# Performance work log

Hardware: AMD Instinct MI355X
Metric: run time of the kernel (lower is better)

The kernel has to match this reference:

```python
import jax, jax.numpy as jnp
import numpy as np

L, B, E, H, HID = 2048, 4, 512, 8, 2048
HD = E // H


def setup_inputs() -> dict:
    key = jax.random.key(0)
    ks = jax.random.split(key, 6)
    s = 0.02
    x = jax.random.normal(ks[0], (L, B, E), jnp.float32)
    in_proj_w = jax.random.normal(ks[1], (3 * E, E), jnp.float32) * s
    in_proj_b = jnp.zeros((3 * E,), jnp.float32)
    out_w = jax.random.normal(ks[2], (E, E), jnp.float32) * s
    out_b = jnp.zeros((E,), jnp.float32)
    w1 = jax.random.normal(ks[3], (HID, E), jnp.float32) * s  # torch Linear: (out, in)
    b1 = jnp.zeros((HID,), jnp.float32)
    w2 = jax.random.normal(ks[4], (E, HID), jnp.float32) * s
    b2 = jnp.zeros((E,), jnp.float32)
    ln_g = jnp.ones((E,), jnp.float32)
    ln_b = jnp.zeros((E,), jnp.float32)
    return {"x": x, "in_proj_w": in_proj_w, "in_proj_b": in_proj_b,
            "out_w": out_w, "out_b": out_b, "w1": w1, "b1": b1,
            "w2": w2, "b2": b2, "ln_g": ln_g, "ln_b": ln_b}


def _pos_encoding(S, Emb, dtype):
    # even i: sin((t+1) * 10000^(-i/E)); odd i: cos((t+1) * 10000^(-(i+1)/E))
    t = jnp.arange(S, dtype=dtype)[:, None]
    i = jnp.arange(Emb, dtype=dtype)[None, :]
    even = jnp.sin((t + 1.0) * jnp.power(10000.0, -i / Emb))
    odd = jnp.cos((t + 1.0) * jnp.power(10000.0, -(i + 1.0) / Emb))
    return jnp.where(jnp.arange(Emb)[None, :] % 2 == 0, even, odd)  # (S, Emb)


def _layernorm(x, g, b, eps=1e-5):
    mu = jnp.mean(x, axis=-1, keepdims=True)
    var = jnp.mean(jnp.square(x - mu), axis=-1, keepdims=True)
    return (x - mu) * jax.lax.rsqrt(var + eps) * g + b


def _mha(x, in_proj_w, in_proj_b, out_w, out_b):
    # x: (L, B, E); self-attention, torch MultiheadAttention semantics
    qkv = jnp.einsum('lbe,fe->lbf', x, in_proj_w) + in_proj_b
    q, k, v = jnp.split(qkv, 3, axis=-1)
    q = q.reshape(L, B, H, HD)
    k = k.reshape(L, B, H, HD)
    v = v.reshape(L, B, H, HD)
    scores = jnp.einsum('lbhd,mbhd->bhlm', q, k) / np.sqrt(HD).astype(np.float32)
    attn = jax.nn.softmax(scores, axis=-1)
    o = jnp.einsum('bhlm,mbhd->lbhd', attn, v).reshape(L, B, E)
    return jnp.einsum('lbe,fe->lbf', o, out_w) + out_b


def reference(x, in_proj_w, in_proj_b, out_w, out_b, w1, b1, w2, b2, ln_g, ln_b):
    # positional encoding: varies along dim1, broadcasts along dim0 (as in source)
    pe = _pos_encoding(x.shape[1], x.shape[2], x.dtype)  # (B, E)
    x = x + pe[None, :, :]
    # Post-Norm path
    x = _layernorm(_mha(x, in_proj_w, in_proj_b, out_w, out_b) + x, ln_g, ln_b)
    h = jax.nn.gelu(jnp.einsum('lbe,he->lbh', x, w1) + b1, approximate=False)
    ff = jnp.einsum('lbh,eh->lbe', h, w2) + b2
    x = _layernorm(ff + x, ln_g, ln_b)
    return x
```

## Files before the change

kernel.cpp:

```cpp
#include <hip/hip_runtime.h>

typedef unsigned short u16;
typedef unsigned int   u32;
typedef u16  u16x2 __attribute__((ext_vector_type(2)));
typedef u16  u16x4 __attribute__((ext_vector_type(4)));
typedef u16  u16x8 __attribute__((ext_vector_type(8)));
typedef short s8v  __attribute__((ext_vector_type(8)));
typedef float f4v  __attribute__((ext_vector_type(4)));
typedef u32  u32x2 __attribute__((ext_vector_type(2)));
typedef u32  u32x4 __attribute__((ext_vector_type(4)));

#define L_SEQ 2048
#define B_SZ  4
#define E_DIM 512
#define H_CNT 8
#define HD    64
#define HID   2048
#define M_ROWS (L_SEQ * B_SZ)
#define QSCALE 0.18033688011112042f

__device__ __forceinline__ u16 f2b(float f) {
    unsigned u = __builtin_bit_cast(unsigned, f);
    u += 0x7fffu + ((u >> 16) & 1u);
    return (u16)(u >> 16);
}
__device__ __forceinline__ float b2f(u16 u) {
    u32 x = ((u32)u) << 16; return __builtin_bit_cast(float, x);
}
#if defined(__has_builtin)
#if __has_builtin(__builtin_amdgcn_cvt_pk_bf16_f32)
#define HAVE_PK_BF16 1
#endif
#if __has_builtin(__builtin_amdgcn_rcpf)
#define HAVE_RCPF 1
#endif
#endif
__device__ __forceinline__ u32 pk_trunc(float a, float b) {
#ifdef HAVE_PK_BF16
    typedef __bf16 bf2 __attribute__((ext_vector_type(2)));
    bf2 r = __builtin_amdgcn_cvt_pk_bf16_f32(a, b);
    return __builtin_bit_cast(u32, r);
#else
    u32 ua = __builtin_bit_cast(u32, a), ub = __builtin_bit_cast(u32, b);
    return (ua >> 16) | (ub & 0xffff0000u);
#endif
}
__device__ __forceinline__ float frcp(float x) {
#ifdef HAVE_RCPF
    return __builtin_amdgcn_rcpf(x);
#else
    return 1.0f / x;
#endif
}
__device__ __forceinline__ void gload_lds16(const u16* g, u16* l) {
    __builtin_amdgcn_global_load_lds((__attribute__((address_space(1))) void*)(u16*)g,
                                     (__attribute__((address_space(3))) void*)l, 16, 0, 0);
}
__device__ __forceinline__ float gelu_f(float v) {
    float y2 = v * (1.5957691216f + 0.0713548576f * v * v);
    return v / (1.0f + __expf(-y2));
}

__global__ __launch_bounds__(256) void pe_tab_k(float* __restrict__ pet) {
    int i = blockIdx.x * 256 + threadIdx.x;
    int e = i & (E_DIM - 1);
    float t = (float)(i >> 9) + 1.0f;
    int ee = (e & 1) ? (e + 1) : e;
    float w = exp2f((-(float)ee / 512.0f) * 13.287712379549449f);
    pet[i] = (e & 1) ? cosf(t * w) : sinf(t * w);
}

__global__ __launch_bounds__(256) void pe_add_k(const float* __restrict__ x,
                                                const float* __restrict__ pet,
                                                u16* __restrict__ xpb) {
    int idx = (blockIdx.x * 256 + threadIdx.x) * 4;
    f4v v = *(const f4v*)(x + idx);
    f4v p = *(const f4v*)(pet + (idx & 2047));
    u16x4 o;
#pragma unroll
    for (int i = 0; i < 4; ++i) o[i] = f2b(v[i] + p[i]);
    *(u16x4*)(xpb + idx) = o;
}

__global__ __launch_bounds__(256) void conv4_k(const float* __restrict__ s1, u16* __restrict__ d1, int n1,
                                               const float* __restrict__ s2, u16* __restrict__ d2, int n2,
                                               const float* __restrict__ s3, u16* __restrict__ d3, int n3,
                                               const float* __restrict__ s4, u16* __restrict__ d4) {
    int o = (blockIdx.x * 256 + threadIdx.x) * 4;
    const float* s; u16* d;
    if (o < n1) { s = s1; d = d1; }
    else { o -= n1;
        if (o < n2) { s = s2; d = d2; }
        else { o -= n2;
            if (o < n3) { s = s3; d = d3; }
            else { o -= n3; s = s4; d = d4; } } }
    f4v v = *(const f4v*)(s + o);
    u16x4 q;
#pragma unroll
    for (int i = 0; i < 4; ++i) q[i] = f2b(v[i]);
    *(u16x4*)(d + o) = q;
}

template <int NP, bool WRITEF, bool WRITEB>
__global__ __launch_bounds__(256)
void ln_c(const u16* __restrict__ p0, const u16* __restrict__ p1,
          const u16* __restrict__ p2, const u16* __restrict__ p3,
          const float* __restrict__ bias, const u16* __restrict__ resid,
          const float* __restrict__ gw, const float* __restrict__ bw,
          float* __restrict__ outF, u16* __restrict__ outB) {
    int wave = threadIdx.x >> 6, lane = threadIdx.x & 63;
    size_t row = (size_t)blockIdx.x * 4 + wave;
    size_t off = row * E_DIM + lane * 8;
    u16x8 rv = *(const u16x8*)(resid + off);
    f4v a, b;
#pragma unroll
    for (int i = 0; i < 4; ++i) { a[i] = b2f(rv[i]); b[i] = b2f(rv[i + 4]); }
    a += *(const f4v*)(bias + lane * 8);
    b += *(const f4v*)(bias + lane * 8 + 4);
    const u16* ps[4] = {p0, p1, p2, p3};
#pragma unroll
    for (int z = 0; z < NP; ++z) {
        u16x8 t = *(const u16x8*)(ps[z] + off);
#pragma unroll
        for (int i = 0; i < 4; ++i) { a[i] += b2f(t[i]); b[i] += b2f(t[i + 4]); }
    }
    float s = (a[0] + a[1]) + (a[2] + a[3]) + (b[0] + b[1]) + (b[2] + b[3]);
#pragma unroll
    for (int o = 1; o < 64; o <<= 1) s += __shfl_xor(s, o, 64);
    float mu = s * (1.0f / E_DIM);
    float q = 0.f;
#pragma unroll
    for (int i = 0; i < 4; ++i) { float d = a[i] - mu; q += d * d; }
#pragma unroll
    for (int i = 0; i < 4; ++i) { float d = b[i] - mu; q += d * d; }
#pragma unroll
    for (int o = 1; o < 64; o <<= 1) q += __shfl_xor(q, o, 64);
    float rstd = rsqrtf(q * (1.0f / E_DIM) + 1e-5f);
    f4v g0 = *(const f4v*)(gw + lane * 8), g1 = *(const f4v*)(gw + lane * 8 + 4);
    f4v w0 = *(const f4v*)(bw + lane * 8), w1 = *(const f4v*)(bw + lane * 8 + 4);
    f4v y0, y1;
#pragma unroll
    for (int i = 0; i < 4; ++i) { y0[i] = (a[i] - mu) * rstd * g0[i] + w0[i];
                                  y1[i] = (b[i] - mu) * rstd * g1[i] + w1[i]; }
    if (WRITEF) {
        *(f4v*)(outF + off)     = y0;
        *(f4v*)(outF + off + 4) = y1;
    }
    if (WRITEB) {
        u16x8 o;
#pragma unroll
        for (int i = 0; i < 4; ++i) { o[i] = f2b(y0[i]); o[i + 4] = f2b(y1[i]); }
        *(u16x8*)(outB + off) = o;
    }
}

__global__ __launch_bounds__(256) void transpose_v_k(const u16* __restrict__ vb,
                                                     u16* __restrict__ vt) {
    __shared__ __align__(16) u16 T[64 * 66];
    int t = threadIdx.x;
    int lt = blockIdx.x, bh = blockIdx.y;
    const u16* src = vb + (size_t)bh * (L_SEQ * HD) + (size_t)lt * 64 * HD;
    int lr = t >> 2, d0 = (t & 3) * 16;
    s8v va = *(const s8v*)(src + lr * HD + d0);
    s8v vb8 = *(const s8v*)(src + lr * HD + d0 + 8);
#pragma unroll
    for (int c = 0; c < 4; ++c) {
        u16x2 p0; p0[0] = (u16)va[c * 2]; p0[1] = (u16)va[c * 2 + 1];
        u16x2 p1; p1[0] = (u16)vb8[c * 2]; p1[1] = (u16)vb8[c * 2 + 1];
        *(u16x2*)(&T[lr * 66 + d0 + c * 2])     = p0;
        *(u16x2*)(&T[lr * 66 + d0 + 8 + c * 2]) = p1;
    }
    __syncthreads();
    int d = t >> 2, l0 = (t & 3) * 16;
    u16 tmp[16];
#pragma unroll
    for (int i = 0; i < 16; ++i) tmp[i] = T[(l0 + i) * 66 + d];
    u16* dst = vt + (size_t)bh * (L_SEQ * HD) + (size_t)d * L_SEQ + lt * 64 + l0;
    u16x8 o0, o1;
#pragma unroll
    for (int i = 0; i < 8; ++i) { o0[i] = tmp[i]; o1[i] = tmp[8 + i]; }
    *(u16x8*)dst       = o0;
    *(u16x8*)(dst + 8) = o1;
}

template <int MODE, int NT>
__global__ __launch_bounds__(256, 4)
void gemm_bt(const u16* __restrict__ A, const u16* __restrict__ Bw,
             const float* __restrict__ bias, int M, int N, int K,
             u16* __restrict__ outB,
             u16* __restrict__ oq, u16* __restrict__ okk, u16* __restrict__ ov) {
    __shared__ __align__(16) u16 As[2][128 * 32];
    __shared__ __align__(16) u16 Bs[2][128 * 32];
    const int tid = threadIdx.x;
    const int wave = tid >> 6, lane = tid & 63;
    const int col = lane & 15, quad = lane >> 4;
    const int n = blockIdx.x;
    const int xcd = n & 7, loc = n >> 3;
    const int mpx = (M / 128) >> 3;
    const int bm = (xcd * mpx + loc / NT) * 128;
    const int bn = (loc % NT) * 128;
    const int wm = (wave >> 1) * 64, wn = (wave & 1) * 64;
    f4v acc[4][4] = {};
    const int srow = wave * 16 + (lane >> 2);
    const int soff = (lane & 3) * 8;
    const u16* Ag = A + (size_t)(bm + srow) * K + soff;
    const u16* Bg = Bw + (size_t)(bn + srow) * K + soff;
    const int wo = wave * 512;
    gload_lds16(Ag,                  &As[0][wo]);
    gload_lds16(Ag + (size_t)64 * K, &As[0][wo + 2048]);
    gload_lds16(Bg,                  &Bs[0][wo]);
    gload_lds16(Bg + (size_t)64 * K, &Bs[0][wo + 2048]);
    const int nit = K >> 5;
    for (int t = 0; t < nit; ++t) {
        const int cur = t & 1, nxt = cur ^ 1;
        __syncthreads();
        if (t + 1 < nit) {
            const int kc = (t + 1) * 32;
            gload_lds16(Ag + kc,                  &As[nxt][wo]);
            gload_lds16(Ag + (size_t)64 * K + kc, &As[nxt][wo + 2048]);
            gload_lds16(Bg + kc,                  &Bs[nxt][wo]);
            gload_lds16(Bg + (size_t)64 * K + kc, &Bs[nxt][wo + 2048]);
        }
        s8v af[4], bf[4];
#pragma unroll
        for (int i = 0; i < 4; ++i) af[i] = *(const s8v*)(&As[cur][(wm + i * 16 + col) * 32 + quad * 8]);
#pragma unroll
        for (int j = 0; j < 4; ++j) bf[j] = *(const s8v*)(&Bs[cur][(wn + j * 16 + col) * 32 + quad * 8]);
#pragma unroll
        for (int i = 0; i < 4; ++i)
#pragma unroll
            for (int j = 0; j < 4; ++j)
                acc[i][j] = __builtin_amdgcn_mfma_f32_16x16x32_bf16(af[i], bf[j], acc[i][j], 0, 0, 0);
    }
#pragma unroll
    for (int j = 0; j < 4; ++j) {
        int gn = bn + wn + j * 16 + col;
        float bv = bias[gn];
        int which = gn >> 9, hh = (gn >> 6) & 7, d = gn & 63;
        u16* dst = (MODE == 0) ? ((which == 0) ? oq : ((which == 1) ? okk : ov)) : outB;
        float qs = (MODE == 0 && which == 0) ? QSCALE : 1.0f;
#pragma unroll
        for (int i = 0; i < 4; ++i) {
            int gm0 = bm + wm + i * 16 + quad * 4;
#pragma unroll
            for (int r = 0; r < 4; ++r) {
                float v = acc[i][j][r] + bv;
                int m = gm0 + r;
                if (MODE == 2) {
                    outB[(size_t)m * N + gn] = f2b(gelu_f(v));
                } else {
                    int l = m >> 2, bb = m & 3;
                    dst[((size_t)(bb * H_CNT + hh) * L_SEQ + l) * HD + d] = f2b(v * qs);
                }
            }
        }
    }
}

__global__ __launch_bounds__(256, 4)
void gemm_ks(const u16* __restrict__ A, const u16* __restrict__ Bw,
             int N, int K, int Kper,
             u16* __restrict__ q0, u16* __restrict__ q1) {
    __shared__ __align__(16) u16 As[2][128 * 32];
    __shared__ __align__(16) u16 Bs[2][128 * 32];
    const int tid = threadIdx.x;
    const int wave = tid >> 6, lane = tid & 63;
    const int col = lane & 15, quad = lane >> 4;
    const int n = blockIdx.x;
    const int xcd = n & 7, loc = n >> 3;
    const int bn = (loc & 3) * 128;
    const int bm = (xcd * 8 + ((loc >> 2) & 7)) * 128;
    const int kz = loc >> 5;
    u16* pz = kz ? q1 : q0;
    const int wm = (wave >> 1) * 64, wn = (wave & 1) * 64;
    f4v acc[4][4] = {};
    const int srow = wave * 16 + (lane >> 2);
    const int soff = (lane & 3) * 8;
    const u16* Ag = A + (size_t)(bm + srow) * K + kz * Kper + soff;
    const u16* Bg = Bw + (size_t)(bn + srow) * K + kz * Kper + soff;
    const int wo = wave * 512;
    gload_lds16(Ag,                  &As[0][wo]);
    gload_lds16(Ag + (size_t)64 * K, &As[0][wo + 2048]);
    gload_lds16(Bg,                  &Bs[0][wo]);
    gload_lds16(Bg + (size_t)64 * K, &Bs[0][wo + 2048]);
    const int nit = Kper >> 5;
    for (int t = 0; t < nit; ++t) {
        const int cur = t & 1, nxt = cur ^ 1;
        __syncthreads();
        if (t + 1 < nit) {
            const int kc = (t + 1) * 32;
            gload_lds16(Ag + kc,                  &As[nxt][wo]);
            gload_lds16(Ag + (size_t)64 * K + kc, &As[nxt][wo + 2048]);
            gload_lds16(Bg + kc,                  &Bs[nxt][wo]);
            gload_lds16(Bg + (size_t)64 * K + kc, &Bs[nxt][wo + 2048]);
        }
        s8v af[4], bf[4];
#pragma unroll
        for (int i = 0; i < 4; ++i) af[i] = *(const s8v*)(&As[cur][(wm + i * 16 + col) * 32 + quad * 8]);
#pragma unroll
        for (int j = 0; j < 4; ++j) bf[j] = *(const s8v*)(&Bs[cur][(wn + j * 16 + col) * 32 + quad * 8]);
#pragma unroll
        for (int i = 0; i < 4; ++i)
#pragma unroll
            for (int j = 0; j < 4; ++j)
                acc[i][j] = __builtin_amdgcn_mfma_f32_16x16x32_bf16(af[i], bf[j], acc[i][j], 0, 0, 0);
    }
#pragma unroll
    for (int j = 0; j < 4; ++j) {
        int gn = bn + wn + j * 16 + col;
#pragma unroll
        for (int i = 0; i < 4; ++i) {
            int m0 = bm + wm + i * 16 + quad * 4;
#pragma unroll
            for (int r = 0; r < 4; ++r)
                pz[(size_t)(m0 + r) * N + gn] = f2b(acc[i][j][r]);
        }
    }
}

__global__ __launch_bounds__(256, 4)
void attn_k(const u16* __restrict__ qg, const u16* __restrict__ kg,
            const u16* __restrict__ vtg, u16* __restrict__ og) {
    __shared__ __align__(16) u16 Ks[2][2][64 * 32];
    __shared__ __align__(16) u16 Vs[2][2][64 * 32];
    const int tid = threadIdx.x;
    const int wave = tid >> 6, lane = tid & 63;
    const int col = lane & 15, quad = lane >> 4;
    const int flat = blockIdx.x;
    const int xcd = flat & 7, loc = flat >> 3;
    const int bh = xcd * 4 + (loc >> 4);
    const int qc = loc & 15;
    const size_t base = (size_t)bh * (L_SEQ * HD);
    s8v qf[2][2];
#pragma unroll
    for (int t = 0; t < 2; ++t) {
        const int qrow = qc * 128 + wave * 32 + t * 16 + col;
#pragma unroll
        for (int hh = 0; hh < 2; ++hh)
            qf[t][hh] = *(const s8v*)(qg + base + (size_t)qrow * HD + hh * 32 + quad * 8);
    }
    f4v oa[2][4] = {};
    f4v la[2] = {};
    const s8v vones8 = {0x3F80, 0x3F80, 0x3F80, 0x3F80, 0x3F80, 0x3F80, 0x3F80, 0x3F80};
    const int h = wave & 1, r0 = (wave >> 1) * 16;
    const int srow = lane >> 2, c = lane & 3;
    const int cp = c ^ ((srow >> 1) & 3);
    const int sig = ((srow >> 2) << 3) + ((r0 >> 4) << 2) + (srow & 3);
    const u16* Kg = kg + base + (size_t)sig * HD + h * 32 + cp * 8;
    const u16* Vg = vtg + base + (size_t)(r0 + srow) * L_SEQ + h * 32 + cp * 8;
    {
        gload_lds16(Kg,                      &Ks[0][h][r0 * 32]);
        gload_lds16(Kg + (size_t)32 * HD,    &Ks[0][h][(r0 + 32) * 32]);
        gload_lds16(Vg,                      &Vs[0][h][r0 * 32]);
        gload_lds16(Vg + (size_t)32 * L_SEQ, &Vs[0][h][(r0 + 32) * 32]);
    }
    const int perm = (col >> 1) & 3;
    for (int it = 0; it < 32; ++it) {
        const int cur = it & 1, nxt = cur ^ 1;
        __syncthreads();
        if (it + 1 < 32) {
            const int kv0 = (it + 1) * 64;
            gload_lds16(Kg + (size_t)kv0 * HD,         &Ks[nxt][h][r0 * 32]);
            gload_lds16(Kg + (size_t)(kv0 + 32) * HD,  &Ks[nxt][h][(r0 + 32) * 32]);
            gload_lds16(Vg + kv0,                      &Vs[nxt][h][r0 * 32]);
            gload_lds16(Vg + kv0 + (size_t)32 * L_SEQ, &Vs[nxt][h][(r0 + 32) * 32]);
        }
        f4v st[2][4];
#pragma unroll
        for (int j = 0; j < 4; ++j) {
            s8v k0 = *(const s8v*)(&Ks[cur][0][(j * 16 + col) * 32 + ((quad ^ perm) * 8)]);
            s8v k1 = *(const s8v*)(&Ks[cur][1][(j * 16 + col) * 32 + ((quad ^ perm) * 8)]);
#pragma unroll
            for (int t = 0; t < 2; ++t) {
                f4v z = {};
                z = __builtin_amdgcn_mfma_f32_16x16x32_bf16(k0, qf[t][0], z, 0, 0, 0);
                z = __builtin_amdgcn_mfma_f32_16x16x32_bf16(k1, qf[t][1], z, 0, 0, 0);
                st[t][j] = z;
            }
        }
        u32 pk[2][4][2];
#pragma unroll
        for (int t = 0; t < 2; ++t)
#pragma unroll
            for (int j = 0; j < 4; ++j) {
                f4v p;
#pragma unroll
                for (int r = 0; r < 4; ++r) p[r] = __builtin_amdgcn_exp2f(st[t][j][r]);
                pk[t][j][0] = pk_trunc(p[0], p[1]);
                pk[t][j][1] = pk_trunc(p[2], p[3]);
            }
#pragma unroll
        for (int c2 = 0; c2 < 2; ++c2) {
            s8v pf[2];
#pragma unroll
            for (int t = 0; t < 2; ++t) {
                u32x4 q4 = {pk[t][2 * c2][0], pk[t][2 * c2][1],
                            pk[t][2 * c2 + 1][0], pk[t][2 * c2 + 1][1]};
                pf[t] = __builtin_bit_cast(s8v, q4);
            }
#pragma unroll
            for (int dj = 0; dj < 4; ++dj) {
                s8v vf = *(const s8v*)(&Vs[cur][c2][(dj * 16 + col) * 32 + ((quad ^ perm) * 8)]);
#pragma unroll
                for (int t = 0; t < 2; ++t)
                    oa[t][dj] = __builtin_amdgcn_mfma_f32_16x16x32_bf16(pf[t], vf, oa[t][dj], 0, 0, 0);
            }
#pragma unroll
            for (int t = 0; t < 2; ++t)
                la[t] = __builtin_amdgcn_mfma_f32_16x16x32_bf16(pf[t], vones8, la[t], 0, 0, 0);
        }
    }
    const int b = bh >> 3, hd = bh & 7;
#pragma unroll
    for (int t = 0; t < 2; ++t)
#pragma unroll
        for (int r = 0; r < 4; ++r) {
            float inv = frcp(la[t][r]);
            int lrow = qc * 128 + wave * 32 + t * 16 + quad * 4 + r;
            size_t mrow = (size_t)(lrow * 4 + b) * E_DIM + hd * HD;
#pragma unroll
            for (int dj = 0; dj < 4; ++dj)
                og[mrow + dj * 16 + col] = f2b(oa[t][dj][r] * inv);
        }
}

extern "C" void kernel_launch(void* const* d_in, const int* in_sizes, int n_in,
                              void* d_out, int out_size, void* d_ws, size_t ws_size,
                              hipStream_t stream) {
    const float* x     = (const float*)d_in[0];
    const float* w_qkv = (const float*)d_in[1];
    const float* b_qkv = (const float*)d_in[2];
    const float* w_out = (const float*)d_in[3];
    const float* b_out = (const float*)d_in[4];
    const float* w1    = (const float*)d_in[5];
    const float* b1    = (const float*)d_in[6];
    const float* w2    = (const float*)d_in[7];
    const float* b2    = (const float*)d_in[8];
    const float* ln_g  = (const float*)d_in[9];
    const float* ln_b  = (const float*)d_in[10];

    char* ws = (char*)d_ws;
    u16*   WQKV = (u16*)(ws + 0);
    u16*   WOUT = (u16*)(ws + 1572864);
    u16*   W1B  = (u16*)(ws + 2097152);
    u16*   W2B  = (u16*)(ws + 4194304);
    u16*   XPB  = (u16*)(ws + 6291456);
    u16*   QB   = (u16*)(ws + 14680064);
    u16*   KB   = (u16*)(ws + 23068672);
    u16*   VB   = (u16*)(ws + 31457280);
    u16*   VT   = (u16*)(ws + 39845888);
    float* PET  = (float*)(ws + 82837504);
    u16*   OB   = VB;
    u16*   OP0  = (u16*)(ws + 48234496);
    u16*   OP1  = (u16*)(ws + 56623104);
    u16*   X3B  = QB;
    u16*   HB   = (u16*)(ws + 48234496);
    u16*   FP0  = XPB;
    u16*   FP1  = KB;

    pe_tab_k<<<8, 256, 0, stream>>>(PET);
    pe_add_k<<<4096, 256, 0, stream>>>(x, PET, XPB);
    conv4_k<<<3072, 256, 0, stream>>>(w_qkv, WQKV, 3 * E_DIM * E_DIM,
                                      w_out, WOUT, E_DIM * E_DIM,
                                      w1, W1B, HID * E_DIM,
                                      w2, W2B);
    gemm_bt<0, 12><<<768, 256, 0, stream>>>(XPB, WQKV, b_qkv, M_ROWS, 3 * E_DIM, E_DIM,
                                            nullptr, QB, KB, VB);
    transpose_v_k<<<dim3(32, 32), 256, 0, stream>>>(VB, VT);
    attn_k<<<512, 256, 0, stream>>>(QB, KB, VT, OB);
    gemm_ks<<<512, 256, 0, stream>>>(OB, WOUT, E_DIM, E_DIM, 256, OP0, OP1);
    ln_c<2, false, true><<<2048, 256, 0, stream>>>(OP0, OP1, nullptr, nullptr,
                                                   b_out, XPB, ln_g, ln_b, nullptr, X3B);
    gemm_bt<2, 16><<<1024, 256, 0, stream>>>(X3B, W1B, b1, M_ROWS, HID, E_DIM,
                                             HB, nullptr, nullptr, nullptr);
    gemm_ks<<<512, 256, 0, stream>>>(HB, W2B, E_DIM, HID, 1024, FP0, FP1);
    ln_c<2, true, false><<<2048, 256, 0, stream>>>(FP0, FP1, nullptr, nullptr,
                                                   b2, X3B, ln_g, ln_b, (float*)d_out, nullptr);
}
```

Before: 248.9 us.

## Load attention K/V fragments directly from global into registers, drop LDS staging

```diff
diff --git a/kernel.cpp b/kernel.cpp
--- a/kernel.cpp
+++ b/kernel.cpp
@@ -318,11 +318,9 @@
     }
 }
 
-__global__ __launch_bounds__(256, 4)
+__global__ __launch_bounds__(256, 2)
 void attn_k(const u16* __restrict__ qg, const u16* __restrict__ kg,
             const u16* __restrict__ vtg, u16* __restrict__ og) {
-    __shared__ __align__(16) u16 Ks[2][2][64 * 32];
-    __shared__ __align__(16) u16 Vs[2][2][64 * 32];
     const int tid = threadIdx.x;
     const int wave = tid >> 6, lane = tid & 63;
     const int col = lane & 15, quad = lane >> 4;
@@ -340,82 +338,101 @@
             qf[t][hh] = *(const s8v*)(qg + base + (size_t)qrow * HD + hh * 32 + quad * 8);
     }
     f4v oa[2][4] = {};
-    f4v la[2] = {};
-    const s8v vones8 = {0x3F80, 0x3F80, 0x3F80, 0x3F80, 0x3F80, 0x3F80, 0x3F80, 0x3F80};
-    const int h = wave & 1, r0 = (wave >> 1) * 16;
-    const int srow = lane >> 2, c = lane & 3;
-    const int cp = c ^ ((srow >> 1) & 3);
-    const int sig = ((srow >> 2) << 3) + ((r0 >> 4) << 2) + (srow & 3);
-    const u16* Kg = kg + base + (size_t)sig * HD + h * 32 + cp * 8;
-    const u16* Vg = vtg + base + (size_t)(r0 + srow) * L_SEQ + h * 32 + cp * 8;
-    {
-        gload_lds16(Kg,                      &Ks[0][h][r0 * 32]);
-        gload_lds16(Kg + (size_t)32 * HD,    &Ks[0][h][(r0 + 32) * 32]);
-        gload_lds16(Vg,                      &Vs[0][h][r0 * 32]);
-        gload_lds16(Vg + (size_t)32 * L_SEQ, &Vs[0][h][(r0 + 32) * 32]);
-    }
-    const int perm = (col >> 1) & 3;
-    for (int it = 0; it < 32; ++it) {
-        const int cur = it & 1, nxt = cur ^ 1;
-        __syncthreads();
-        if (it + 1 < 32) {
-            const int kv0 = (it + 1) * 64;
-            gload_lds16(Kg + (size_t)kv0 * HD,         &Ks[nxt][h][r0 * 32]);
-            gload_lds16(Kg + (size_t)(kv0 + 32) * HD,  &Ks[nxt][h][(r0 + 32) * 32]);
-            gload_lds16(Vg + kv0,                      &Vs[nxt][h][r0 * 32]);
-            gload_lds16(Vg + kv0 + (size_t)32 * L_SEQ, &Vs[nxt][h][(r0 + 32) * 32]);
-        }
-        f4v st[2][4];
-#pragma unroll
-        for (int j = 0; j < 4; ++j) {
-            s8v k0 = *(const s8v*)(&Ks[cur][0][(j * 16 + col) * 32 + ((quad ^ perm) * 8)]);
-            s8v k1 = *(const s8v*)(&Ks[cur][1][(j * 16 + col) * 32 + ((quad ^ perm) * 8)]);
-#pragma unroll
-            for (int t = 0; t < 2; ++t) {
-                f4v z = {};
-                z = __builtin_amdgcn_mfma_f32_16x16x32_bf16(k0, qf[t][0], z, 0, 0, 0);
-                z = __builtin_amdgcn_mfma_f32_16x16x32_bf16(k1, qf[t][1], z, 0, 0, 0);
-                st[t][j] = z;
-            }
-        }
-        u32 pk[2][4][2];
-#pragma unroll
-        for (int t = 0; t < 2; ++t)
-#pragma unroll
-            for (int j = 0; j < 4; ++j) {
-                f4v p;
-#pragma unroll
-                for (int r = 0; r < 4; ++r) p[r] = __builtin_amdgcn_exp2f(st[t][j][r]);
-                pk[t][j][0] = pk_trunc(p[0], p[1]);
-                pk[t][j][1] = pk_trunc(p[2], p[3]);
-            }
-#pragma unroll
-        for (int c2 = 0; c2 < 2; ++c2) {
-            s8v pf[2];
-#pragma unroll
-            for (int t = 0; t < 2; ++t) {
-                u32x4 q4 = {pk[t][2 * c2][0], pk[t][2 * c2][1],
-                            pk[t][2 * c2 + 1][0], pk[t][2 * c2 + 1][1]};
-                pf[t] = __builtin_bit_cast(s8v, q4);
-            }
-#pragma unroll
-            for (int dj = 0; dj < 4; ++dj) {
-                s8v vf = *(const s8v*)(&Vs[cur][c2][(dj * 16 + col) * 32 + ((quad ^ perm) * 8)]);
-#pragma unroll
-                for (int t = 0; t < 2; ++t)
-                    oa[t][dj] = __builtin_amdgcn_mfma_f32_16x16x32_bf16(pf[t], vf, oa[t][dj], 0, 0, 0);
-            }
-#pragma unroll
-            for (int t = 0; t < 2; ++t)
-                la[t] = __builtin_amdgcn_mfma_f32_16x16x32_bf16(pf[t], vones8, la[t], 0, 0, 0);
-        }
-    }
+    float ls0 = 0.f, ls1 = 0.f;
+    const u16* kr[4];
+#pragma unroll
+    for (int j = 0; j < 4; ++j) {
+        int sig = 32 * (j >> 1) + 8 * (col >> 2) + 4 * (j & 1) + (col & 3);
+        kr[j] = kg + base + (size_t)sig * HD + quad * 8;
+    }
+    const u16* vr[2][4];
+#pragma unroll
+    for (int c2 = 0; c2 < 2; ++c2)
+#pragma unroll
+        for (int dj = 0; dj < 4; ++dj)
+            vr[c2][dj] = vtg + base + (size_t)(dj * 16 + col) * L_SEQ + c2 * 32 + quad * 8;
+
+    s8v kfA[4][2], kfB[4][2];
+#pragma unroll
+    for (int j = 0; j < 4; ++j) {
+        kfA[j][0] = *(const s8v*)(kr[j]);
+        kfA[j][1] = *(const s8v*)(kr[j] + 32);
+    }
+
+#define ATTN_STEP(KF_CUR, KF_NXT, KOFF, VOFF)                                              \
+    {                                                                                      \
+        s8v vf0[4], vf1[4];                                                                \
+        _Pragma("unroll")                                                                  \
+        for (int dj = 0; dj < 4; ++dj) {                                                   \
+            vf0[dj] = *(const s8v*)(vr[0][dj] + (VOFF));                                   \
+            vf1[dj] = *(const s8v*)(vr[1][dj] + (VOFF));                                   \
+        }                                                                                  \
+        _Pragma("unroll")                                                                  \
+        for (int j = 0; j < 4; ++j) {                                                      \
+            KF_NXT[j][0] = *(const s8v*)(kr[j] + (KOFF));                                  \
+            KF_NXT[j][1] = *(const s8v*)(kr[j] + (KOFF) + 32);                             \
+        }                                                                                  \
+        f4v st[2][4];                                                                      \
+        _Pragma("unroll")                                                                  \
+        for (int j = 0; j < 4; ++j) {                                                      \
+            _Pragma("unroll")                                                              \
+            for (int t = 0; t < 2; ++t) {                                                  \
+                f4v z = {};                                                                \
+                z = __builtin_amdgcn_mfma_f32_16x16x32_bf16(KF_CUR[j][0], qf[t][0], z, 0, 0, 0); \
+                z = __builtin_amdgcn_mfma_f32_16x16x32_bf16(KF_CUR[j][1], qf[t][1], z, 0, 0, 0); \
+                st[t][j] = z;                                                              \
+            }                                                                              \
+        }                                                                                  \
+        u32 pk[2][4][2];                                                                   \
+        _Pragma("unroll")                                                                  \
+        for (int t = 0; t < 2; ++t)                                                        \
+            _Pragma("unroll")                                                              \
+            for (int j = 0; j < 4; ++j) {                                                  \
+                f4v p;                                                                     \
+                _Pragma("unroll")                                                          \
+                for (int r = 0; r < 4; ++r) p[r] = __builtin_amdgcn_exp2f(st[t][j][r]);    \
+                float psum = (p[0] + p[1]) + (p[2] + p[3]);                                \
+                if (t == 0) ls0 += psum; else ls1 += psum;                                 \
+                pk[t][j][0] = pk_trunc(p[0], p[1]);                                        \
+                pk[t][j][1] = pk_trunc(p[2], p[3]);                                        \
+            }                                                                              \
+        _Pragma("unroll")                                                                  \
+        for (int c2 = 0; c2 < 2; ++c2) {                                                   \
+            s8v pf[2];                                                                     \
+            _Pragma("unroll")                                                              \
+            for (int t = 0; t < 2; ++t) {                                                  \
+                u32x4 q4 = {pk[t][2 * c2][0], pk[t][2 * c2][1],                            \
+                            pk[t][2 * c2 + 1][0], pk[t][2 * c2 + 1][1]};                   \
+                pf[t] = __builtin_bit_cast(s8v, q4);                                       \
+            }                                                                              \
+            _Pragma("unroll")                                                              \
+            for (int dj = 0; dj < 4; ++dj) {                                               \
+                s8v vf = (c2 == 0) ? vf0[dj] : vf1[dj];                                    \
+                _Pragma("unroll")                                                          \
+                for (int t = 0; t < 2; ++t)                                                \
+                    oa[t][dj] = __builtin_amdgcn_mfma_f32_16x16x32_bf16(pf[t], vf, oa[t][dj], 0, 0, 0); \
+            }                                                                              \
+        }                                                                                  \
+    }
+
+    for (int it = 0; it < 32; it += 2) {
+        const size_t ko1 = (size_t)(it + 1) * (64 * HD);
+        const size_t ko2 = (size_t)((it + 2) < 32 ? (it + 2) : 0) * (64 * HD);
+        const size_t vo1 = (size_t)it * 64, vo2 = (size_t)(it + 1) * 64;
+        ATTN_STEP(kfA, kfB, ko1, vo1);
+        ATTN_STEP(kfB, kfA, ko2, vo2);
+    }
+#undef ATTN_STEP
+
+    ls0 += __shfl_xor(ls0, 16, 64); ls0 += __shfl_xor(ls0, 32, 64);
+    ls1 += __shfl_xor(ls1, 16, 64); ls1 += __shfl_xor(ls1, 32, 64);
     const int b = bh >> 3, hd = bh & 7;
 #pragma unroll
     for (int t = 0; t < 2; ++t)
 #pragma unroll
         for (int r = 0; r < 4; ++r) {
-            float inv = frcp(la[t][r]);
+            float lv = __shfl(t == 0 ? ls0 : ls1, quad * 4 + r, 64);
+            float inv = frcp(lv);
             int lrow = qc * 128 + wave * 32 + t * 16 + quad * 4 + r;
             size_t mrow = (size_t)(lrow * 4 + b) * E_DIM + hd * HD;
 #pragma unroll
```

Result: slower. 325.8 us (+30.9%).

## Halve attention block size and replace ones-MFMA row sums with shuffles

Applied to the files above, without the earlier changes.

```diff
diff --git a/kernel.cpp b/kernel.cpp
--- a/kernel.cpp
+++ b/kernel.cpp
@@ -318,7 +318,7 @@
     }
 }
 
-__global__ __launch_bounds__(256, 4)
+__global__ __launch_bounds__(128, 2)
 void attn_k(const u16* __restrict__ qg, const u16* __restrict__ kg,
             const u16* __restrict__ vtg, u16* __restrict__ og) {
     __shared__ __align__(16) u16 Ks[2][2][64 * 32];
@@ -328,31 +328,36 @@
     const int col = lane & 15, quad = lane >> 4;
     const int flat = blockIdx.x;
     const int xcd = flat & 7, loc = flat >> 3;
-    const int bh = xcd * 4 + (loc >> 4);
-    const int qc = loc & 15;
+    const int bh = xcd * 4 + (loc >> 5);
+    const int qc = loc & 31;
     const size_t base = (size_t)bh * (L_SEQ * HD);
     s8v qf[2][2];
 #pragma unroll
     for (int t = 0; t < 2; ++t) {
-        const int qrow = qc * 128 + wave * 32 + t * 16 + col;
+        const int qrow = qc * 64 + wave * 32 + t * 16 + col;
 #pragma unroll
         for (int hh = 0; hh < 2; ++hh)
             qf[t][hh] = *(const s8v*)(qg + base + (size_t)qrow * HD + hh * 32 + quad * 8);
     }
     f4v oa[2][4] = {};
-    f4v la[2] = {};
-    const s8v vones8 = {0x3F80, 0x3F80, 0x3F80, 0x3F80, 0x3F80, 0x3F80, 0x3F80, 0x3F80};
-    const int h = wave & 1, r0 = (wave >> 1) * 16;
+    float ls0 = 0.f, ls1 = 0.f;
+    const int h = wave;
     const int srow = lane >> 2, c = lane & 3;
     const int cp = c ^ ((srow >> 1) & 3);
-    const int sig = ((srow >> 2) << 3) + ((r0 >> 4) << 2) + (srow & 3);
-    const u16* Kg = kg + base + (size_t)sig * HD + h * 32 + cp * 8;
-    const u16* Vg = vtg + base + (size_t)(r0 + srow) * L_SEQ + h * 32 + cp * 8;
+    const u16* Kg[4];
+    const u16* Vg[4];
+#pragma unroll
+    for (int z = 0; z < 4; ++z) {
+        const int sig = 32 * (z >> 1) + 4 * (z & 1) + 8 * (srow >> 2) + (srow & 3);
+        Kg[z] = kg + base + (size_t)sig * HD + h * 32 + cp * 8;
+        Vg[z] = vtg + base + (size_t)(z * 16 + srow) * L_SEQ + h * 32 + cp * 8;
+    }
     {
-        gload_lds16(Kg,                      &Ks[0][h][r0 * 32]);
-        gload_lds16(Kg + (size_t)32 * HD,    &Ks[0][h][(r0 + 32) * 32]);
-        gload_lds16(Vg,                      &Vs[0][h][r0 * 32]);
-        gload_lds16(Vg + (size_t)32 * L_SEQ, &Vs[0][h][(r0 + 32) * 32]);
+#pragma unroll
+        for (int z = 0; z < 4; ++z) {
+            gload_lds16(Kg[z], &Ks[0][h][(z * 16) * 32]);
+            gload_lds16(Vg[z], &Vs[0][h][(z * 16) * 32]);
+        }
     }
     const int perm = (col >> 1) & 3;
     for (int it = 0; it < 32; ++it) {
@@ -360,10 +365,11 @@
         __syncthreads();
         if (it + 1 < 32) {
             const int kv0 = (it + 1) * 64;
-            gload_lds16(Kg + (size_t)kv0 * HD,         &Ks[nxt][h][r0 * 32]);
-            gload_lds16(Kg + (size_t)(kv0 + 32) * HD,  &Ks[nxt][h][(r0 + 32) * 32]);
-            gload_lds16(Vg + kv0,                      &Vs[nxt][h][r0 * 32]);
-            gload_lds16(Vg + kv0 + (size_t)32 * L_SEQ, &Vs[nxt][h][(r0 + 32) * 32]);
+#pragma unroll
+            for (int z = 0; z < 4; ++z) {
+                gload_lds16(Kg[z] + (size_t)kv0 * HD, &Ks[nxt][h][(z * 16) * 32]);
+                gload_lds16(Vg[z] + kv0,              &Vs[nxt][h][(z * 16) * 32]);
+            }
         }
         f4v st[2][4];
 #pragma unroll
@@ -386,6 +392,8 @@
                 f4v p;
 #pragma unroll
                 for (int r = 0; r < 4; ++r) p[r] = __builtin_amdgcn_exp2f(st[t][j][r]);
+                float psum = (p[0] + p[1]) + (p[2] + p[3]);
+                if (t == 0) ls0 += psum; else ls1 += psum;
                 pk[t][j][0] = pk_trunc(p[0], p[1]);
                 pk[t][j][1] = pk_trunc(p[2], p[3]);
             }
@@ -405,18 +413,18 @@
                 for (int t = 0; t < 2; ++t)
                     oa[t][dj] = __builtin_amdgcn_mfma_f32_16x16x32_bf16(pf[t], vf, oa[t][dj], 0, 0, 0);
             }
-#pragma unroll
-            for (int t = 0; t < 2; ++t)
-                la[t] = __builtin_amdgcn_mfma_f32_16x16x32_bf16(pf[t], vones8, la[t], 0, 0, 0);
-        }
-    }
+        }
+    }
+    ls0 += __shfl_xor(ls0, 16, 64); ls0 += __shfl_xor(ls0, 32, 64);
+    ls1 += __shfl_xor(ls1, 16, 64); ls1 += __shfl_xor(ls1, 32, 64);
     const int b = bh >> 3, hd = bh & 7;
 #pragma unroll
     for (int t = 0; t < 2; ++t)
 #pragma unroll
         for (int r = 0; r < 4; ++r) {
-            float inv = frcp(la[t][r]);
-            int lrow = qc * 128 + wave * 32 + t * 16 + quad * 4 + r;
+            float lv = __shfl(t == 0 ? ls0 : ls1, quad * 4 + r, 64);
+            float inv = frcp(lv);
+            int lrow = qc * 64 + wave * 32 + t * 16 + quad * 4 + r;
             size_t mrow = (size_t)(lrow * 4 + b) * E_DIM + hd * HD;
 #pragma unroll
             for (int dj = 0; dj < 4; ++dj)
@@ -467,7 +475,7 @@
     gemm_bt<0, 12><<<768, 256, 0, stream>>>(XPB, WQKV, b_qkv, M_ROWS, 3 * E_DIM, E_DIM,
                                             nullptr, QB, KB, VB);
     transpose_v_k<<<dim3(32, 32), 256, 0, stream>>>(VB, VT);
-    attn_k<<<512, 256, 0, stream>>>(QB, KB, VT, OB);
+    attn_k<<<1024, 128, 0, stream>>>(QB, KB, VT, OB);
     gemm_ks<<<512, 256, 0, stream>>>(OB, WOUT, E_DIM, E_DIM, 256, OP0, OP1);
     ln_c<2, false, true><<<2048, 256, 0, stream>>>(OP0, OP1, nullptr, nullptr,
                                                    b_out, XPB, ln_g, ln_b, nullptr, X3B);
```

Measured after the change: 251.8 us. No clear change (+1.2%).
